# Performance work log

Measured on AMD Instinct MI355X. Metric: run time of the kernel, lower is better.

The kernel has to match this reference:

```python
import jax, jax.numpy as jnp
import numpy as np
from jax import lax

N_STEPS = 8          # fixed-step discretization of t in [0, 1]
GN_GROUPS = 32       # group_norm(width) -> GroupNorm(min(32, width), width)
GN_EPS = 1e-5

# Tsit5 Butcher tableau (c nodes, a stage coeffs, b solution weights; b7 = 0)
_C = (0.161, 0.327, 0.9, 0.9800255409045097, 1.0)
_A = (
    (0.161,),
    (-0.008480655492356989, 0.335480655492357),
    (2.8971530571054935, -6.359448489975075, 4.3622954328695815),
    (5.325864828439257, -11.748883564062828, 7.4955393428898365, -0.09249506636175525),
    (5.86145544294642, -12.92096931784711, 8.159367898576159, -0.071584973281401, -0.028269050394068383),
)
_B = (0.09646076681806523, 0.01, 0.4798896504144996, 1.379008574103742, -3.290069515436081, 2.324710524099774)


def _conv3x3(x, w, b):
    # x: [B, Cin, H, W], w: [Cout, Cin, 3, 3], padding=1, stride=1
    y = lax.conv_general_dilated(x, w, (1, 1), ((1, 1), (1, 1)),
                                 dimension_numbers=("NCHW", "OIHW", "NCHW"))
    return y + b[None, :, None, None]


def _group_norm(x, scale, bias):
    B, C, H, W = x.shape
    xr = x.reshape(B, GN_GROUPS, C // GN_GROUPS, H, W)
    mu = xr.mean(axis=(2, 3, 4), keepdims=True)
    var = xr.var(axis=(2, 3, 4), keepdims=True)
    xn = ((xr - mu) * lax.rsqrt(var + GN_EPS)).reshape(B, C, H, W)
    return xn * scale[None, :, None, None] + bias[None, :, None, None]


def _ode_func(t, x, p):
    # ConcatConv2D: prepend a channel filled with scalar t
    B, _, H, W = x.shape
    tt = jnp.full((B, 1, H, W), t, dtype=x.dtype)
    h = _conv3x3(jnp.concatenate([tt, x], axis=1), p["conv1_w"], p["conv1_b"])
    h = jax.nn.relu(_group_norm(h, p["gn1_scale"], p["gn1_bias"]))
    tt2 = jnp.full((B, 1, H, W), t, dtype=x.dtype)
    h = _conv3x3(jnp.concatenate([tt2, h], axis=1), p["conv2_w"], p["conv2_b"])
    return _group_norm(h, p["gn2_scale"], p["gn2_bias"])


def _tsit5_solve(x, p):
    dt = jnp.float32(1.0 / N_STEPS)

    def step(carry, _):
        y, t = carry
        k1 = _ode_func(t, y, p)
        k2 = _ode_func(t + _C[0] * dt, y + dt * (_A[0][0] * k1), p)
        k3 = _ode_func(t + _C[1] * dt, y + dt * (_A[1][0] * k1 + _A[1][1] * k2), p)
        k4 = _ode_func(t + _C[2] * dt,
                       y + dt * (_A[2][0] * k1 + _A[2][1] * k2 + _A[2][2] * k3), p)
        k5 = _ode_func(t + _C[3] * dt,
                       y + dt * (_A[3][0] * k1 + _A[3][1] * k2 + _A[3][2] * k3 + _A[3][3] * k4), p)
        k6 = _ode_func(t + _C[4] * dt,
                       y + dt * (_A[4][0] * k1 + _A[4][1] * k2 + _A[4][2] * k3
                                 + _A[4][3] * k4 + _A[4][4] * k5), p)
        y_next = y + dt * (_B[0] * k1 + _B[1] * k2 + _B[2] * k3
                           + _B[3] * k4 + _B[4] * k5 + _B[5] * k6)
        return (y_next, t + dt), None

    (yT, _), _ = lax.scan(step, (x, jnp.float32(0.0)), None, length=N_STEPS)
    return yT


def setup_inputs() -> dict:
    key = jax.random.key(0)
    ks = jax.random.split(key, 5)
    B, C, H, W = 64, 64, 32, 32
    cin = C + 1  # concat t channel
    fan_in = cin * 9
    lim = 1.0 / np.sqrt(fan_in)
    x = jax.random.normal(ks[0], (B, C, H, W), dtype=jnp.float32)
    conv1_w = jax.random.uniform(ks[1], (C, cin, 3, 3), jnp.float32, -lim, lim)
    conv1_b = jax.random.uniform(ks[2], (C,), jnp.float32, -lim, lim)
    conv2_w = jax.random.uniform(ks[3], (C, cin, 3, 3), jnp.float32, -lim, lim)
    conv2_b = jax.random.uniform(ks[4], (C,), jnp.float32, -lim, lim)
    return {
        "x": x,
        "conv1_w": conv1_w, "conv1_b": conv1_b,
        "gn1_scale": jnp.ones((C,), jnp.float32), "gn1_bias": jnp.zeros((C,), jnp.float32),
        "conv2_w": conv2_w, "conv2_b": conv2_b,
        "gn2_scale": jnp.ones((C,), jnp.float32), "gn2_bias": jnp.zeros((C,), jnp.float32),
    }


def reference(x, conv1_w, conv1_b, gn1_scale, gn1_bias, conv2_w, conv2_b, gn2_scale, gn2_bias):
    p = {"conv1_w": conv1_w, "conv1_b": conv1_b, "gn1_scale": gn1_scale, "gn1_bias": gn1_bias,
         "conv2_w": conv2_w, "conv2_b": conv2_b, "gn2_scale": gn2_scale, "gn2_bias": gn2_bias}
    return _tsit5_solve(x, p)
```

## Files before the change

kernel.cpp:

```cpp
#include <hip/hip_runtime.h>

typedef __attribute__((ext_vector_type(8))) _Float16 f16x8;
typedef __attribute__((ext_vector_type(4))) float f32x4;
typedef unsigned short u16;

#define BB 64
#define NPIX 1024
#define NELEM (BB*64*NPIX)
#define NRT 8

#define PLANE (6*34*64)

__device__ __forceinline__ int swz8(int c8, int p) {
    return (c8 + ((p + (p >> 2)) & 7)) & 7;
}

__device__ __forceinline__ u16 f2h(float x) {
    _Float16 h = (_Float16)x;
    return __builtin_bit_cast(u16, h);
}
__device__ __forceinline__ float h2f(u16 u) {
    return (float)__builtin_bit_cast(_Float16, u);
}

__global__ __launch_bounds__(256) void prep_w_k(
    const float* __restrict__ w, u16* __restrict__ wt)
{
    int t = blockIdx.x*256 + threadIdx.x;
    if (t >= 4608) return;
    int lane = t & 63;
    int f = t >> 6;
    int g = f & 7;
    int tap = f >> 3;
    int coutblk = g & 3;
    int kc = g >> 2;
    int cout = coutblk*16 + (lane & 15);
    int quad = lane >> 4;
    u16 v[8];
#pragma unroll
    for (int j = 0; j < 8; ++j) {
        int cin = kc*32 + quad*8 + j;
        v[j] = f2h(w[((size_t)cout*65 + (cin+1))*9 + tap]);
    }
    u16* dst = wt + ((size_t)tap*4096 + (g*64 + lane)*8);
    *(ushort4*)(dst)     = make_ushort4(v[0], v[1], v[2], v[3]);
    *(ushort4*)(dst + 4) = make_ushort4(v[4], v[5], v[6], v[7]);
}

__global__ __launch_bounds__(256) void smap_k(
    const float* __restrict__ w, float* __restrict__ smap)
{
    int t = blockIdx.x*256 + threadIdx.x;
    int cout = t >> 10;
    int pix = t & 1023;
    int y = pix >> 5, x = pix & 31;
    float s = 0.f;
#pragma unroll
    for (int dy = 0; dy < 3; ++dy)
#pragma unroll
        for (int dx = 0; dx < 3; ++dx) {
            int yy = y + dy - 1, xx = x + dx - 1;
            if ((unsigned)yy < 32u && (unsigned)xx < 32u)
                s += w[(size_t)cout*65*9 + dy*3 + dx];
        }
    smap[t] = s;
}

__global__ __launch_bounds__(512, 4) void conv_mfma_k(
    const float* __restrict__ src0, const u16* __restrict__ srcb,
    const u16* __restrict__ kp0, const u16* __restrict__ kp1,
    const u16* __restrict__ kp2, const u16* __restrict__ kp3,
    const u16* __restrict__ kp4,
    float* __restrict__ part,
    const float* __restrict__ gns, const float* __restrict__ gnb,
    const float* __restrict__ gks, const float* __restrict__ gkb,
    const u16* __restrict__ wt, const float* __restrict__ smap,
    const float* __restrict__ bias, u16* __restrict__ out, float tval,
    int mode, int nk, int slot_in, int slot_out,
    float a1, float a2, float a3, float a4, float a5)
{
    __shared__ u16 lds_in[PLANE];
    __shared__ float kaf[5][64];
    __shared__ float kbf[64];
    __shared__ float sgA[5][64];
    __shared__ float ps[256], pss[256];
    __shared__ float rg[64], rgq[64];

    const int rt  = blockIdx.x;
    const int b   = blockIdx.y;
    const int tid = threadIdx.x;
    const int wv   = tid >> 6;
    const int lane = tid & 63;
    const int quad = lane >> 4;
    const int n15  = lane & 15;
    const int r0   = wv & 3;
    const int mh   = wv >> 2;

    if (mode == 2) {
        if (tid < 64) {
            int g = tid & 31, st = tid >> 5;
            const float* pp = part + ((((size_t)slot_in*64 + b)*32 + g)*NRT)*2 + st;
            float v = 0.f;
#pragma unroll
            for (int q = 0; q < NRT; ++q) v += pp[2*q];
            sgA[0][st*32+g] = v;
        }
        __syncthreads();
        if (tid < 64) {
            int g = tid >> 1;
            float mu   = sgA[0][g] * (1.f/2048.f);
            float var  = sgA[0][32+g] * (1.f/2048.f) - mu*mu;
            float rstd = rsqrtf(var + 1e-5f);
            float a = gns[tid]*rstd;
            kaf[0][tid] = a;
            kbf[tid] = gnb[tid] - mu*a;
        }
    } else if (mode == 1) {
        if (tid < 64) {
            int g = tid & 31, st = tid >> 5;
            for (int jj = 0; jj < nk; ++jj) {
                const float* pp = part + ((((size_t)(1+jj)*64 + b)*32 + g)*NRT)*2 + st;
                float v = 0.f;
#pragma unroll
                for (int q = 0; q < NRT; ++q) v += pp[2*q];
                sgA[jj][st*32+g] = v;
            }
        }
        __syncthreads();
        if (tid < 64) {
            const float aa[5] = {a1, a2, a3, a4, a5};
            int g = tid >> 1;
            float acb = 0.f;
            for (int jj = 0; jj < nk; ++jj) {
                float mu   = sgA[jj][g] * (1.f/2048.f);
                float var  = sgA[jj][32+g] * (1.f/2048.f) - mu*mu;
                float rstd = rsqrtf(var + 1e-5f);
                float a = gks[tid]*rstd;
                float c = gkb[tid] - mu*a;
                kaf[jj][tid] = aa[jj]*a;
                acb += aa[jj]*c;
            }
            kbf[tid] = acb;
        }
    } else {
        if (tid < 64) { kaf[0][tid] = 1.f; kbf[tid] = 0.f; }
    }
    __syncthreads();

#pragma unroll
    for (int i = 0; i < 3; ++i) {
        int u  = tid + i*512;
        int q4 = u & 7;
        int t2 = u >> 3;
        int rr = t2 % 6;
        int c2 = t2 / 6;
        int gr = rt*4 + rr - 1;
        bool ok = (unsigned)gr < 32u;
        int ch0 = c2*2, ch1 = ch0 + 1;
        float4 a0 = make_float4(0.f,0.f,0.f,0.f), a1v = a0;
        if (ok) {
            const size_t base = (((size_t)b*64 + ch0)*32 + gr)*32 + q4*4;
            if (mode == 2) {
                ushort4 H0 = *(const ushort4*)(srcb + base);
                ushort4 H1 = *(const ushort4*)(srcb + base + 1024);
                float A0 = kaf[0][ch0], B0 = kbf[ch0];
                float A1 = kaf[0][ch1], B1 = kbf[ch1];
                a0.x = fmaxf(fmaf(h2f(H0.x),A0,B0), 0.f);
                a0.y = fmaxf(fmaf(h2f(H0.y),A0,B0), 0.f);
                a0.z = fmaxf(fmaf(h2f(H0.z),A0,B0), 0.f);
                a0.w = fmaxf(fmaf(h2f(H0.w),A0,B0), 0.f);
                a1v.x = fmaxf(fmaf(h2f(H1.x),A1,B1), 0.f);
                a1v.y = fmaxf(fmaf(h2f(H1.y),A1,B1), 0.f);
                a1v.z = fmaxf(fmaf(h2f(H1.z),A1,B1), 0.f);
                a1v.w = fmaxf(fmaf(h2f(H1.w),A1,B1), 0.f);
            } else {
                a0  = *(const float4*)(src0 + base);
                a1v = *(const float4*)(src0 + base + 1024);
                if (mode == 1) {
                    float f0 = kbf[ch0], f1 = kbf[ch1];
                    a0.x += f0; a0.y += f0; a0.z += f0; a0.w += f0;
                    a1v.x += f1; a1v.y += f1; a1v.z += f1; a1v.w += f1;
                    const u16* kps[5] = {kp0, kp1, kp2, kp3, kp4};
#pragma unroll
                    for (int jj = 0; jj < 5; ++jj) {
                        if (jj >= nk) break;
                        ushort4 kv0 = *(const ushort4*)(kps[jj] + base);
                        ushort4 kv1 = *(const ushort4*)(kps[jj] + base + 1024);
                        float fa0 = kaf[jj][ch0], fa1 = kaf[jj][ch1];
                        a0.x = fmaf(fa0, h2f(kv0.x), a0.x);
                        a0.y = fmaf(fa0, h2f(kv0.y), a0.y);
                        a0.z = fmaf(fa0, h2f(kv0.z), a0.z);
                        a0.w = fmaf(fa0, h2f(kv0.w), a0.w);
                        a1v.x = fmaf(fa1, h2f(kv1.x), a1v.x);
                        a1v.y = fmaf(fa1, h2f(kv1.y), a1v.y);
                        a1v.z = fmaf(fa1, h2f(kv1.z), a1v.z);
                        a1v.w = fmaf(fa1, h2f(kv1.w), a1v.w);
                    }
                }
            }
        }
        float v0[4] = {a0.x, a0.y, a0.z, a0.w};
        float v1[4] = {a1v.x, a1v.y, a1v.z, a1v.w};
        int c8 = c2 >> 2, cl = c2 & 3;
        int pbase = rr*34 + 1 + q4*4;
#pragma unroll
        for (int j = 0; j < 4; ++j) {
            int p = pbase + j;
            int au = p*64 + swz8(c8, p)*8 + cl*2;
            *(unsigned*)&lds_in[au] =
                (unsigned)f2h(v0[j]) | ((unsigned)f2h(v1[j]) << 16);
        }
    }
    if (tid < 384) {
        int c2 = tid & 31;
        int t3 = tid >> 5;
        int rr = t3 % 6;
        int e  = t3 / 6;
        int p  = rr*34 + e*33;
        int au = p*64 + swz8(c2 >> 2, p)*8 + (c2 & 3)*2;
        *(unsigned*)&lds_in[au] = 0u;
    }
    __syncthreads();

    f32x4 acc[2][2] = {};
#pragma unroll 3
    for (int tap = 0; tap < 9; ++tap) {
        const int dy = tap / 3;
        const int dx = tap - dy*3;
        const int rowoff = (r0 + dy)*34 + dx;
        const u16* wtap = wt + (size_t)tap*4096;
#pragma unroll
        for (int kc = 0; kc < 2; ++kc) {
            f16x8 A[2], Bf[2];
#pragma unroll
            for (int mt = 0; mt < 2; ++mt)
                A[mt] = *(const f16x8*)
                    &wtap[((kc*4 + mh*2 + mt)*64 + lane)*8];
#pragma unroll
            for (int nt = 0; nt < 2; ++nt) {
                int p = rowoff + nt*16 + n15;
                Bf[nt] = *(const f16x8*)&lds_in[p*64 + swz8(kc*4 + quad, p)*8];
            }
#pragma unroll
            for (int mt = 0; mt < 2; ++mt)
#pragma unroll
                for (int nt = 0; nt < 2; ++nt)
                    acc[mt][nt] = __builtin_amdgcn_mfma_f32_16x16x32_f16(
                        A[mt], Bf[nt], acc[mt][nt], 0, 0, 0);
        }
    }

    const int orow = rt*4 + r0;
#pragma unroll
    for (int mt = 0; mt < 2; ++mt) {
#pragma unroll
        for (int r = 0; r < 4; ++r) {
            int cout = mh*32 + mt*16 + quad*4 + r;
            float bs = bias[cout];
            const float* sp = smap + (size_t)cout*1024 + orow*32;
            u16* op = out + (((size_t)b*64 + cout)*32 + orow)*32;
            float v0 = acc[mt][0][r] + bs + tval*sp[n15];
            float v1 = acc[mt][1][r] + bs + tval*sp[16 + n15];
            op[n15]      = f2h(v0);
            op[16 + n15] = f2h(v1);
            float s = v0 + v1;
            float q = v0*v0 + v1*v1;
            s += __shfl_xor(s, 1); q += __shfl_xor(q, 1);
            s += __shfl_xor(s, 2); q += __shfl_xor(q, 2);
            s += __shfl_xor(s, 4); q += __shfl_xor(q, 4);
            s += __shfl_xor(s, 8); q += __shfl_xor(q, 8);
            if (n15 == 0) { ps[r0*64 + cout] = s; pss[r0*64 + cout] = q; }
        }
    }
    __syncthreads();
    if (tid < 64) {
        rg[tid]  = ps[tid]  + ps[64+tid]  + ps[128+tid]  + ps[192+tid];
        rgq[tid] = pss[tid] + pss[64+tid] + pss[128+tid] + pss[192+tid];
    }
    __syncthreads();
    if (tid < 32) {
        float S  = rg[2*tid]  + rg[2*tid+1];
        float SS = rgq[2*tid] + rgq[2*tid+1];
        float* pp = part + ((((size_t)slot_out*64 + b)*32 + tid)*NRT + rt)*2;
        pp[0] = S; pp[1] = SS;
    }
}

__global__ __launch_bounds__(256) void final_combine_k(
    float* __restrict__ y,
    const u16* __restrict__ k0, const u16* __restrict__ k1,
    const u16* __restrict__ k2, const u16* __restrict__ k3,
    const u16* __restrict__ k4, const u16* __restrict__ k5,
    const float* __restrict__ part,
    const float* __restrict__ g2s, const float* __restrict__ g2b,
    float b0, float b1, float b2, float b3, float b4, float b5)
{
    const int bidx = blockIdx.x;
    const int b = bidx >> 6, ch = bidx & 63, g = ch >> 1;
    const int t = threadIdx.x;
    __shared__ float rs[6][2];
    if (t < 12) {
        int jj = t >> 1, st = t & 1;
        const float* pp = part + ((((size_t)(1+jj)*64 + b)*32 + g)*NRT)*2 + st;
        float v = 0.f;
#pragma unroll
        for (int q = 0; q < NRT; ++q) v += pp[2*q];
        rs[jj][st] = v;
    }
    __syncthreads();
    const float bb[6] = {b0, b1, b2, b3, b4, b5};
    float fa[6], fcs = 0.f;
#pragma unroll
    for (int jj = 0; jj < 6; ++jj) {
        float mu   = rs[jj][0] * (1.f/2048.f);
        float var  = rs[jj][1] * (1.f/2048.f) - mu*mu;
        float rstd = rsqrtf(var + 1e-5f);
        float a = g2s[ch]*rstd;
        float c = g2b[ch] - mu*a;
        fa[jj] = bb[jj]*a;
        fcs   += bb[jj]*c;
    }
    const size_t base = ((size_t)bidx*256 + t)*4;
    float4 r = *(const float4*)(y + base);
    r.x += fcs; r.y += fcs; r.z += fcs; r.w += fcs;
    const u16* kp[6] = {k0, k1, k2, k3, k4, k5};
#pragma unroll
    for (int jj = 0; jj < 6; ++jj) {
        ushort4 kv = *(const ushort4*)(kp[jj] + base);
        r.x = fmaf(fa[jj], h2f(kv.x), r.x);
        r.y = fmaf(fa[jj], h2f(kv.y), r.y);
        r.z = fmaf(fa[jj], h2f(kv.z), r.z);
        r.w = fmaf(fa[jj], h2f(kv.w), r.w);
    }
    *(float4*)(y + base) = r;
}


static const double A_[5][5] = {
    {0.161, 0, 0, 0, 0},
    {-0.008480655492356989, 0.335480655492357, 0, 0, 0},
    {2.8971530571054935, -6.359448489975075, 4.3622954328695815, 0, 0},
    {5.325864828439257, -11.748883564062828, 7.4955393428898365, -0.09249506636175525, 0},
    {5.86145544294642, -12.92096931784711, 8.159367898576159, -0.071584973281401, -0.028269050394068383},
};
static const double B_[6] = {
    0.09646076681806523, 0.01, 0.4798896504144996,
    1.379008574103742, -3.290069515436081, 2.324710524099774,
};
static const double C_[5] = {0.161, 0.327, 0.9, 0.9800255409045097, 1.0};

extern "C" void kernel_launch(void* const* d_in, const int* in_sizes, int n_in,
                              void* d_out, int out_size, void* d_ws, size_t ws_size,
                              hipStream_t stream)
{
    const float* x   = (const float*)d_in[0];
    const float* c1w = (const float*)d_in[1];
    const float* c1b = (const float*)d_in[2];
    const float* g1s = (const float*)d_in[3];
    const float* g1b = (const float*)d_in[4];
    const float* c2w = (const float*)d_in[5];
    const float* c2b = (const float*)d_in[6];
    const float* g2s = (const float*)d_in[7];
    const float* g2b = (const float*)d_in[8];

    float* y  = (float*)d_out;
    u16*   wsb = (u16*)d_ws;
    u16*   h  = wsb;
    u16*   k[6];
    for (int i = 0; i < 6; ++i) k[i] = wsb + (size_t)(1 + i) * NELEM;
    u16*   wt1   = wsb + (size_t)7*NELEM;
    u16*   wt2   = wt1 + 73728;
    float* smap1 = (float*)(wt2 + 73728);
    float* smap2 = smap1 + 65536;
    float* part  = smap2 + 65536;

    const double dt = 0.125;
    const float dtf = 0.125f;

    prep_w_k<<<18, 256, 0, stream>>>(c1w, wt1);
    prep_w_k<<<18, 256, 0, stream>>>(c2w, wt2);
    smap_k<<<256, 256, 0, stream>>>(c1w, smap1);
    smap_k<<<256, 256, 0, stream>>>(c2w, smap2);

    hipMemcpyAsync(y, x, (size_t)NELEM * sizeof(float),
                   hipMemcpyDeviceToDevice, stream);

    const dim3 cgrid(NRT, BB);

    for (int s = 0; s < 8; ++s) {
        const float t0 = dtf * (float)s;
        for (int j = 0; j < 6; ++j) {
            const float tj = (j == 0) ? t0 : t0 + (float)C_[j-1] * dtf;
            float a[5] = {0,0,0,0,0};
            for (int i = 0; i < j; ++i) a[i] = (float)(A_[j-1][i] * dt);
            conv_mfma_k<<<cgrid, 512, 0, stream>>>(
                y, nullptr, k[0], k[1], k[2], k[3], k[4],
                part, g1s, g1b, g2s, g2b,
                wt1, smap1, c1b, h, tj,
                (j == 0) ? 0 : 1, j, 0, 0,
                a[0], a[1], a[2], a[3], a[4]);
            conv_mfma_k<<<cgrid, 512, 0, stream>>>(
                nullptr, h, nullptr, nullptr, nullptr, nullptr, nullptr,
                part, g1s, g1b, g2s, g2b,
                wt2, smap2, c2b, k[j], tj,
                2, 0, 0, 1 + j,
                0.f, 0.f, 0.f, 0.f, 0.f);
        }
        final_combine_k<<<4096, 256, 0, stream>>>(
            y, k[0], k[1], k[2], k[3], k[4], k[5], part, g2s, g2b,
            (float)(B_[0]*dt), (float)(B_[1]*dt), (float)(B_[2]*dt),
            (float)(B_[3]*dt), (float)(B_[4]*dt), (float)(B_[5]*dt));
    }
}
```

Before: 2.104 ms.

## Fuse step combine into next conv, template modes, split-K prefetch overlap

Templates the conv kernel on mode, stage count and a write-y flag so the branches and the stage-count loop are resolved at compile time. The per-step final combine is folded into the first conv of the next step, which rebuilds y from the previous y and the six k buffers and writes it to a ping-pong buffer. This removes a separate full-tensor pass per step. The input staging is split into two channel halves so the global loads for the second half are issued while the MFMAs run on the first half. The GroupNorm partial reduction is simplified to vectorized float4 loads with no extra sync. The cost is more kernel instantiations, extra workspace for two y buffers, and higher register pressure from the prefetched values.

```diff
diff --git a/kernel.cpp b/kernel.cpp
--- a/kernel.cpp
+++ b/kernel.cpp
@@ -66,23 +66,24 @@
     smap[t] = s;
 }
 
+template<int MODE, int NK, bool WRITEY>
 __global__ __launch_bounds__(512, 4) void conv_mfma_k(
     const float* __restrict__ src0, const u16* __restrict__ srcb,
     const u16* __restrict__ kp0, const u16* __restrict__ kp1,
     const u16* __restrict__ kp2, const u16* __restrict__ kp3,
-    const u16* __restrict__ kp4,
+    const u16* __restrict__ kp4, const u16* __restrict__ kp5,
+    float* __restrict__ yout,
     float* __restrict__ part,
     const float* __restrict__ gns, const float* __restrict__ gnb,
     const float* __restrict__ gks, const float* __restrict__ gkb,
     const u16* __restrict__ wt, const float* __restrict__ smap,
     const float* __restrict__ bias, u16* __restrict__ out, float tval,
-    int mode, int nk, int slot_in, int slot_out,
-    float a1, float a2, float a3, float a4, float a5)
+    int slot_in, int slot_out,
+    float a1, float a2, float a3, float a4, float a5, float a6)
 {
     __shared__ u16 lds_in[PLANE];
-    __shared__ float kaf[5][64];
+    __shared__ float kaf[6][64];
     __shared__ float kbf[64];
-    __shared__ float sgA[5][64];
     __shared__ float ps[256], pss[256];
     __shared__ float rg[64], rgq[64];
 
@@ -96,44 +97,147 @@
     const int r0   = wv & 3;
     const int mh   = wv >> 2;
 
-    if (mode == 2) {
+    float4 Y0[2], Y1[2];
+    ushort4 H0[2], H1[2];
+
+    auto prim_load = [&](int h) {
+#pragma unroll
+        for (int uu = 0; uu < 2; ++uu) {
+            int ur = tid + uu*512;
+            if (ur >= 768) continue;
+            int u = h*768 + ur;
+            int q4 = u & 7;
+            int t2 = u >> 3;
+            int rr = t2 % 6;
+            int c2 = t2 / 6;
+            int gr = rt*4 + rr - 1;
+            if ((unsigned)gr < 32u) {
+                const size_t base = (((size_t)b*64 + c2*2)*32 + gr)*32 + q4*4;
+                if constexpr (MODE == 2) {
+                    H0[uu] = *(const ushort4*)(srcb + base);
+                    H1[uu] = *(const ushort4*)(srcb + base + 1024);
+                } else {
+                    Y0[uu] = *(const float4*)(src0 + base);
+                    Y1[uu] = *(const float4*)(src0 + base + 1024);
+                }
+            }
+        }
+    };
+
+    auto stage_finish = [&](int h) {
+#pragma unroll
+        for (int uu = 0; uu < 2; ++uu) {
+            int ur = tid + uu*512;
+            if (ur >= 768) continue;
+            int u = h*768 + ur;
+            int q4 = u & 7;
+            int t2 = u >> 3;
+            int rr = t2 % 6;
+            int c2 = t2 / 6;
+            int gr = rt*4 + rr - 1;
+            bool ok = (unsigned)gr < 32u;
+            int ch0 = c2*2, ch1 = ch0 + 1;
+            float4 a0 = make_float4(0.f,0.f,0.f,0.f), a1v = a0;
+            if (ok) {
+                const size_t base = (((size_t)b*64 + ch0)*32 + gr)*32 + q4*4;
+                if constexpr (MODE == 2) {
+                    float A0 = kaf[0][ch0], B0 = kbf[ch0];
+                    float A1 = kaf[0][ch1], B1 = kbf[ch1];
+                    a0.x = fmaxf(fmaf(h2f(H0[uu].x),A0,B0), 0.f);
+                    a0.y = fmaxf(fmaf(h2f(H0[uu].y),A0,B0), 0.f);
+                    a0.z = fmaxf(fmaf(h2f(H0[uu].z),A0,B0), 0.f);
+                    a0.w = fmaxf(fmaf(h2f(H0[uu].w),A0,B0), 0.f);
+                    a1v.x = fmaxf(fmaf(h2f(H1[uu].x),A1,B1), 0.f);
+                    a1v.y = fmaxf(fmaf(h2f(H1[uu].y),A1,B1), 0.f);
+                    a1v.z = fmaxf(fmaf(h2f(H1[uu].z),A1,B1), 0.f);
+                    a1v.w = fmaxf(fmaf(h2f(H1[uu].w),A1,B1), 0.f);
+                } else {
+                    a0 = Y0[uu]; a1v = Y1[uu];
+                    if constexpr (MODE == 1) {
+                        float f0 = kbf[ch0], f1 = kbf[ch1];
+                        a0.x += f0; a0.y += f0; a0.z += f0; a0.w += f0;
+                        a1v.x += f1; a1v.y += f1; a1v.z += f1; a1v.w += f1;
+                        const u16* kps[6] = {kp0, kp1, kp2, kp3, kp4, kp5};
+#pragma unroll
+                        for (int jj = 0; jj < NK; ++jj) {
+                            ushort4 kv0 = *(const ushort4*)(kps[jj] + base);
+                            ushort4 kv1 = *(const ushort4*)(kps[jj] + base + 1024);
+                            float fa0 = kaf[jj][ch0], fa1 = kaf[jj][ch1];
+                            a0.x = fmaf(fa0, h2f(kv0.x), a0.x);
+                            a0.y = fmaf(fa0, h2f(kv0.y), a0.y);
+                            a0.z = fmaf(fa0, h2f(kv0.z), a0.z);
+                            a0.w = fmaf(fa0, h2f(kv0.w), a0.w);
+                            a1v.x = fmaf(fa1, h2f(kv1.x), a1v.x);
+                            a1v.y = fmaf(fa1, h2f(kv1.y), a1v.y);
+                            a1v.z = fmaf(fa1, h2f(kv1.z), a1v.z);
+                            a1v.w = fmaf(fa1, h2f(kv1.w), a1v.w);
+                        }
+                    }
+                }
+                if constexpr (WRITEY) {
+                    if (rr >= 1 && rr <= 4) {
+                        *(float4*)(yout + base)        = a0;
+                        *(float4*)(yout + base + 1024) = a1v;
+                    }
+                }
+            }
+            float v0[4] = {a0.x, a0.y, a0.z, a0.w};
+            float v1[4] = {a1v.x, a1v.y, a1v.z, a1v.w};
+            int c8 = c2 >> 2, cl = c2 & 3;
+            int pbase = rr*34 + 1 + q4*4;
+#pragma unroll
+            for (int j = 0; j < 4; ++j) {
+                int p = pbase + j;
+                int au = p*64 + swz8(c8, p)*8 + cl*2;
+                *(unsigned*)&lds_in[au] =
+                    (unsigned)f2h(v0[j]) | ((unsigned)f2h(v1[j]) << 16);
+            }
+        }
+    };
+
+    f32x4 acc[2][2] = {};
+    auto mfma_kc = [&](int kc) {
+#pragma unroll 3
+        for (int tap = 0; tap < 9; ++tap) {
+            const int dy = tap / 3;
+            const int dx = tap - dy*3;
+            const int rowoff = (r0 + dy)*34 + dx;
+            const u16* wtap = wt + (size_t)tap*4096;
+            f16x8 A[2], Bf[2];
+#pragma unroll
+            for (int mt = 0; mt < 2; ++mt)
+                A[mt] = *(const f16x8*)
+                    &wtap[((kc*4 + mh*2 + mt)*64 + lane)*8];
+#pragma unroll
+            for (int nt = 0; nt < 2; ++nt) {
+                int p = rowoff + nt*16 + n15;
+                Bf[nt] = *(const f16x8*)&lds_in[p*64 + swz8(kc*4 + quad, p)*8];
+            }
+#pragma unroll
+            for (int mt = 0; mt < 2; ++mt)
+#pragma unroll
+                for (int nt = 0; nt < 2; ++nt)
+                    acc[mt][nt] = __builtin_amdgcn_mfma_f32_16x16x32_f16(
+                        A[mt], Bf[nt], acc[mt][nt], 0, 0, 0);
+        }
+    };
+
+    prim_load(0);
+
+    if constexpr (MODE == 1) {
         if (tid < 64) {
-            int g = tid & 31, st = tid >> 5;
-            const float* pp = part + ((((size_t)slot_in*64 + b)*32 + g)*NRT)*2 + st;
-            float v = 0.f;
-#pragma unroll
-            for (int q = 0; q < NRT; ++q) v += pp[2*q];
-            sgA[0][st*32+g] = v;
-        }
-        __syncthreads();
-        if (tid < 64) {
-            int g = tid >> 1;
-            float mu   = sgA[0][g] * (1.f/2048.f);
-            float var  = sgA[0][32+g] * (1.f/2048.f) - mu*mu;
-            float rstd = rsqrtf(var + 1e-5f);
-            float a = gns[tid]*rstd;
-            kaf[0][tid] = a;
-            kbf[tid] = gnb[tid] - mu*a;
-        }
-    } else if (mode == 1) {
-        if (tid < 64) {
-            int g = tid & 31, st = tid >> 5;
-            for (int jj = 0; jj < nk; ++jj) {
-                const float* pp = part + ((((size_t)(1+jj)*64 + b)*32 + g)*NRT)*2 + st;
-                float v = 0.f;
-#pragma unroll
-                for (int q = 0; q < NRT; ++q) v += pp[2*q];
-                sgA[jj][st*32+g] = v;
-            }
-        }
-        __syncthreads();
-        if (tid < 64) {
-            const float aa[5] = {a1, a2, a3, a4, a5};
+            const float aa[6] = {a1, a2, a3, a4, a5, a6};
             int g = tid >> 1;
             float acb = 0.f;
-            for (int jj = 0; jj < nk; ++jj) {
-                float mu   = sgA[jj][g] * (1.f/2048.f);
-                float var  = sgA[jj][32+g] * (1.f/2048.f) - mu*mu;
+#pragma unroll
+            for (int jj = 0; jj < NK; ++jj) {
+                const float4* pp = (const float4*)
+                    (part + ((((size_t)(1+jj)*64 + b)*32 + g)*NRT)*2);
+                float4 x0 = pp[0], x1 = pp[1], x2 = pp[2], x3 = pp[3];
+                float S  = x0.x+x0.z + x1.x+x1.z + x2.x+x2.z + x3.x+x3.z;
+                float SS = x0.y+x0.w + x1.y+x1.w + x2.y+x2.w + x3.y+x3.w;
+                float mu   = S * (1.f/2048.f);
+                float var  = SS * (1.f/2048.f) - mu*mu;
                 float rstd = rsqrtf(var + 1e-5f);
                 float a = gks[tid]*rstd;
                 float c = gkb[tid] - mu*a;
@@ -142,75 +246,25 @@
             }
             kbf[tid] = acb;
         }
-    } else {
-        if (tid < 64) { kaf[0][tid] = 1.f; kbf[tid] = 0.f; }
-    }
-    __syncthreads();
-
-#pragma unroll
-    for (int i = 0; i < 3; ++i) {
-        int u  = tid + i*512;
-        int q4 = u & 7;
-        int t2 = u >> 3;
-        int rr = t2 % 6;
-        int c2 = t2 / 6;
-        int gr = rt*4 + rr - 1;
-        bool ok = (unsigned)gr < 32u;
-        int ch0 = c2*2, ch1 = ch0 + 1;
-        float4 a0 = make_float4(0.f,0.f,0.f,0.f), a1v = a0;
-        if (ok) {
-            const size_t base = (((size_t)b*64 + ch0)*32 + gr)*32 + q4*4;
-            if (mode == 2) {
-                ushort4 H0 = *(const ushort4*)(srcb + base);
-                ushort4 H1 = *(const ushort4*)(srcb + base + 1024);
-                float A0 = kaf[0][ch0], B0 = kbf[ch0];
-                float A1 = kaf[0][ch1], B1 = kbf[ch1];
-                a0.x = fmaxf(fmaf(h2f(H0.x),A0,B0), 0.f);
-                a0.y = fmaxf(fmaf(h2f(H0.y),A0,B0), 0.f);
-                a0.z = fmaxf(fmaf(h2f(H0.z),A0,B0), 0.f);
-                a0.w = fmaxf(fmaf(h2f(H0.w),A0,B0), 0.f);
-                a1v.x = fmaxf(fmaf(h2f(H1.x),A1,B1), 0.f);
-                a1v.y = fmaxf(fmaf(h2f(H1.y),A1,B1), 0.f);
-                a1v.z = fmaxf(fmaf(h2f(H1.z),A1,B1), 0.f);
-                a1v.w = fmaxf(fmaf(h2f(H1.w),A1,B1), 0.f);
-            } else {
-                a0  = *(const float4*)(src0 + base);
-                a1v = *(const float4*)(src0 + base + 1024);
-                if (mode == 1) {
-                    float f0 = kbf[ch0], f1 = kbf[ch1];
-                    a0.x += f0; a0.y += f0; a0.z += f0; a0.w += f0;
-                    a1v.x += f1; a1v.y += f1; a1v.z += f1; a1v.w += f1;
-                    const u16* kps[5] = {kp0, kp1, kp2, kp3, kp4};
-#pragma unroll
-                    for (int jj = 0; jj < 5; ++jj) {
-                        if (jj >= nk) break;
-                        ushort4 kv0 = *(const ushort4*)(kps[jj] + base);
-                        ushort4 kv1 = *(const ushort4*)(kps[jj] + base + 1024);
-                        float fa0 = kaf[jj][ch0], fa1 = kaf[jj][ch1];
-                        a0.x = fmaf(fa0, h2f(kv0.x), a0.x);
-                        a0.y = fmaf(fa0, h2f(kv0.y), a0.y);
-                        a0.z = fmaf(fa0, h2f(kv0.z), a0.z);
-                        a0.w = fmaf(fa0, h2f(kv0.w), a0.w);
-                        a1v.x = fmaf(fa1, h2f(kv1.x), a1v.x);
-                        a1v.y = fmaf(fa1, h2f(kv1.y), a1v.y);
-                        a1v.z = fmaf(fa1, h2f(kv1.z), a1v.z);
-                        a1v.w = fmaf(fa1, h2f(kv1.w), a1v.w);
-                    }
-                }
-            }
-        }
-        float v0[4] = {a0.x, a0.y, a0.z, a0.w};
-        float v1[4] = {a1v.x, a1v.y, a1v.z, a1v.w};
-        int c8 = c2 >> 2, cl = c2 & 3;
-        int pbase = rr*34 + 1 + q4*4;
-#pragma unroll
-        for (int j = 0; j < 4; ++j) {
-            int p = pbase + j;
-            int au = p*64 + swz8(c8, p)*8 + cl*2;
-            *(unsigned*)&lds_in[au] =
-                (unsigned)f2h(v0[j]) | ((unsigned)f2h(v1[j]) << 16);
-        }
-    }
+    } else if constexpr (MODE == 2) {
+        if (tid < 64) {
+            int g = tid >> 1;
+            const float4* pp = (const float4*)
+                (part + ((((size_t)slot_in*64 + b)*32 + g)*NRT)*2);
+            float4 x0 = pp[0], x1 = pp[1], x2 = pp[2], x3 = pp[3];
+            float S  = x0.x+x0.z + x1.x+x1.z + x2.x+x2.z + x3.x+x3.z;
+            float SS = x0.y+x0.w + x1.y+x1.w + x2.y+x2.w + x3.y+x3.w;
+            float mu   = S * (1.f/2048.f);
+            float var  = SS * (1.f/2048.f) - mu*mu;
+            float rstd = rsqrtf(var + 1e-5f);
+            float a = gns[tid]*rstd;
+            kaf[0][tid] = a;
+            kbf[tid] = gnb[tid] - mu*a;
+        }
+    }
+    __syncthreads();
+
+    stage_finish(0);
     if (tid < 384) {
         int c2 = tid & 31;
         int t3 = tid >> 5;
@@ -222,33 +276,12 @@
     }
     __syncthreads();
 
-    f32x4 acc[2][2] = {};
-#pragma unroll 3
-    for (int tap = 0; tap < 9; ++tap) {
-        const int dy = tap / 3;
-        const int dx = tap - dy*3;
-        const int rowoff = (r0 + dy)*34 + dx;
-        const u16* wtap = wt + (size_t)tap*4096;
-#pragma unroll
-        for (int kc = 0; kc < 2; ++kc) {
-            f16x8 A[2], Bf[2];
-#pragma unroll
-            for (int mt = 0; mt < 2; ++mt)
-                A[mt] = *(const f16x8*)
-                    &wtap[((kc*4 + mh*2 + mt)*64 + lane)*8];
-#pragma unroll
-            for (int nt = 0; nt < 2; ++nt) {
-                int p = rowoff + nt*16 + n15;
-                Bf[nt] = *(const f16x8*)&lds_in[p*64 + swz8(kc*4 + quad, p)*8];
-            }
-#pragma unroll
-            for (int mt = 0; mt < 2; ++mt)
-#pragma unroll
-                for (int nt = 0; nt < 2; ++nt)
-                    acc[mt][nt] = __builtin_amdgcn_mfma_f32_16x16x32_f16(
-                        A[mt], Bf[nt], acc[mt][nt], 0, 0, 0);
-        }
-    }
+    prim_load(1);
+    mfma_kc(0);
+    stage_finish(1);
+    __syncthreads();
+
+    mfma_kc(1);
 
     const int orow = rt*4 + r0;
 #pragma unroll
@@ -287,7 +320,7 @@
 }
 
 __global__ __launch_bounds__(256) void final_combine_k(
-    float* __restrict__ y,
+    const float* __restrict__ ysrc, float* __restrict__ ydst,
     const u16* __restrict__ k0, const u16* __restrict__ k1,
     const u16* __restrict__ k2, const u16* __restrict__ k3,
     const u16* __restrict__ k4, const u16* __restrict__ k5,
@@ -321,7 +354,7 @@
         fcs   += bb[jj]*c;
     }
     const size_t base = ((size_t)bidx*256 + t)*4;
-    float4 r = *(const float4*)(y + base);
+    float4 r = *(const float4*)(ysrc + base);
     r.x += fcs; r.y += fcs; r.z += fcs; r.w += fcs;
     const u16* kp[6] = {k0, k1, k2, k3, k4, k5};
 #pragma unroll
@@ -332,7 +365,7 @@
         r.z = fmaf(fa[jj], h2f(kv.z), r.z);
         r.w = fmaf(fa[jj], h2f(kv.w), r.w);
     }
-    *(float4*)(y + base) = r;
+    *(float4*)(ydst + base) = r;
 }
 
 
@@ -373,6 +406,9 @@
     float* smap1 = (float*)(wt2 + 73728);
     float* smap2 = smap1 + 65536;
     float* part  = smap2 + 65536;
+    float* YA    = part + (size_t)7*64*32*8*2;
+    float* YB    = YA + NELEM;
+    float* yb[2] = {YA, YB};
 
     const double dt = 0.125;
     const float dtf = 0.125f;
@@ -382,33 +418,81 @@
     smap_k<<<256, 256, 0, stream>>>(c1w, smap1);
     smap_k<<<256, 256, 0, stream>>>(c2w, smap2);
 
-    hipMemcpyAsync(y, x, (size_t)NELEM * sizeof(float),
+    hipMemcpyAsync(YA, x, (size_t)NELEM * sizeof(float),
                    hipMemcpyDeviceToDevice, stream);
 
     const dim3 cgrid(NRT, BB);
+    const float bw0 = (float)(B_[0]*dt), bw1 = (float)(B_[1]*dt),
+                bw2 = (float)(B_[2]*dt), bw3 = (float)(B_[3]*dt),
+                bw4 = (float)(B_[4]*dt), bw5 = (float)(B_[5]*dt);
 
     for (int s = 0; s < 8; ++s) {
         const float t0 = dtf * (float)s;
-        for (int j = 0; j < 6; ++j) {
-            const float tj = (j == 0) ? t0 : t0 + (float)C_[j-1] * dtf;
+        const float* ys = yb[s & 1];
+
+        if (s == 0) {
+            conv_mfma_k<0,0,false><<<cgrid, 512, 0, stream>>>(
+                YA, nullptr, nullptr,nullptr,nullptr,nullptr,nullptr,nullptr,
+                nullptr, part, g1s, g1b, g2s, g2b,
+                wt1, smap1, c1b, h, t0, 0, 0,
+                0.f,0.f,0.f,0.f,0.f,0.f);
+        } else {
+            conv_mfma_k<1,6,true><<<cgrid, 512, 0, stream>>>(
+                yb[(s-1)&1], nullptr, k[0],k[1],k[2],k[3],k[4],k[5],
+                yb[s&1], part, g1s, g1b, g2s, g2b,
+                wt1, smap1, c1b, h, t0, 0, 0,
+                bw0, bw1, bw2, bw3, bw4, bw5);
+        }
+        conv_mfma_k<2,0,false><<<cgrid, 512, 0, stream>>>(
+            nullptr, h, nullptr,nullptr,nullptr,nullptr,nullptr,nullptr,
+            nullptr, part, g1s, g1b, g2s, g2b,
+            wt2, smap2, c2b, k[0], t0, 0, 1,
+            0.f,0.f,0.f,0.f,0.f,0.f);
+
+        for (int j = 1; j < 6; ++j) {
+            const float tj = t0 + (float)C_[j-1] * dtf;
             float a[5] = {0,0,0,0,0};
             for (int i = 0; i < j; ++i) a[i] = (float)(A_[j-1][i] * dt);
-            conv_mfma_k<<<cgrid, 512, 0, stream>>>(
-                y, nullptr, k[0], k[1], k[2], k[3], k[4],
-                part, g1s, g1b, g2s, g2b,
-                wt1, smap1, c1b, h, tj,
-                (j == 0) ? 0 : 1, j, 0, 0,
-                a[0], a[1], a[2], a[3], a[4]);
-            conv_mfma_k<<<cgrid, 512, 0, stream>>>(
-                nullptr, h, nullptr, nullptr, nullptr, nullptr, nullptr,
-                part, g1s, g1b, g2s, g2b,
-                wt2, smap2, c2b, k[j], tj,
-                2, 0, 0, 1 + j,
-                0.f, 0.f, 0.f, 0.f, 0.f);
-        }
-        final_combine_k<<<4096, 256, 0, stream>>>(
-            y, k[0], k[1], k[2], k[3], k[4], k[5], part, g2s, g2b,
-            (float)(B_[0]*dt), (float)(B_[1]*dt), (float)(B_[2]*dt),
-            (float)(B_[3]*dt), (float)(B_[4]*dt), (float)(B_[5]*dt));
-    }
-}
+            switch (j) {
+            case 1:
+                conv_mfma_k<1,1,false><<<cgrid, 512, 0, stream>>>(
+                    ys, nullptr, k[0],k[1],k[2],k[3],k[4],k[5],
+                    nullptr, part, g1s, g1b, g2s, g2b,
+                    wt1, smap1, c1b, h, tj, 0, 0,
+                    a[0],a[1],a[2],a[3],a[4],0.f); break;
+            case 2:
+                conv_mfma_k<1,2,false><<<cgrid, 512, 0, stream>>>(
+                    ys, nullptr, k[0],k[1],k[2],k[3],k[4],k[5],
+                    nullptr, part, g1s, g1b, g2s, g2b,
+                    wt1, smap1, c1b, h, tj, 0, 0,
+                    a[0],a[1],a[2],a[3],a[4],0.f); break;
+            case 3:
+                conv_mfma_k<1,3,false><<<cgrid, 512, 0, stream>>>(
+                    ys, nullptr, k[0],k[1],k[2],k[3],k[4],k[5],
+                    nullptr, part, g1s, g1b, g2s, g2b,
+                    wt1, smap1, c1b, h, tj, 0, 0,
+                    a[0],a[1],a[2],a[3],a[4],0.f); break;
+            case 4:
+                conv_mfma_k<1,4,false><<<cgrid, 512, 0, stream>>>(
+                    ys, nullptr, k[0],k[1],k[2],k[3],k[4],k[5],
+                    nullptr, part, g1s, g1b, g2s, g2b,
+                    wt1, smap1, c1b, h, tj, 0, 0,
+                    a[0],a[1],a[2],a[3],a[4],0.f); break;
+            default:
+                conv_mfma_k<1,5,false><<<cgrid, 512, 0, stream>>>(
+                    ys, nullptr, k[0],k[1],k[2],k[3],k[4],k[5],
+                    nullptr, part, g1s, g1b, g2s, g2b,
+                    wt1, smap1, c1b, h, tj, 0, 0,
+                    a[0],a[1],a[2],a[3],a[4],0.f); break;
+            }
+            conv_mfma_k<2,0,false><<<cgrid, 512, 0, stream>>>(
+                nullptr, h, nullptr,nullptr,nullptr,nullptr,nullptr,nullptr,
+                nullptr, part, g1s, g1b, g2s, g2b,
+                wt2, smap2, c2b, k[j], tj, 0, 1 + j,
+                0.f,0.f,0.f,0.f,0.f,0.f);
+        }
+    }
+    final_combine_k<<<4096, 256, 0, stream>>>(
+        yb[7 & 1], y, k[0], k[1], k[2], k[3], k[4], k[5], part, g2s, g2b,
+        bw0, bw1, bw2, bw3, bw4, bw5);
+}
```

Result: faster. 1.835 ms (-12.8%).
